# Optimization experiments

Measured on AMD Instinct MI355X. Metric: run time of the kernel, lower is better.

## Reference

```python
import jax, jax.numpy as jnp
import numpy as np

B = 262144
D = 16
G = 20000


def setup_inputs() -> dict:
    key = jax.random.key(0)
    ks = jax.random.split(key, 20)
    lin = lambda k, o, i: jax.random.normal(k, (o, i), jnp.float32) * (1.0 / np.sqrt(i))
    inp = {
        "x": jax.random.randint(ks[0], (B, 2), 0, G),
        "phenos": jax.random.normal(ks[1], (B, 2), jnp.float32),
        "emb": jax.random.normal(ks[2], (G, D), jnp.float32),
        "W1": lin(ks[3], D, D), "b1": jnp.zeros((D,), jnp.float32),
        "W2": lin(ks[4], D, D), "b2": jnp.zeros((D,), jnp.float32),
        "W3": lin(ks[5], D, D), "b3": jnp.zeros((D,), jnp.float32),
        # bilinear weights: small noise + stacked identity, as in the torch init
        "BW": 0.01 * jax.random.normal(ks[6], (D, D, D), jnp.float32)
              + jnp.broadcast_to(jnp.eye(D, dtype=jnp.float32)[None, :, :], (D, D, D)),
        "BD": 0.01 * jax.random.normal(ks[7], (D, D), jnp.float32) + 1.0,
        "Boff": 0.01 * jax.random.normal(ks[8], (D,), jnp.float32),
        "Wc1": lin(ks[9], D, D), "bc1": jnp.zeros((D,), jnp.float32),
        "Wc2": lin(ks[10], 1, D), "bc2": jnp.zeros((1,), jnp.float32),
    }
    return inp


def reference(x, phenos, emb, W1, b1, W2, b2, W3, b3, BW, BD, Boff, Wc1, bc1, Wc2, bc2):
    # embedding lookup: [B, 2, D] -> flatten gene axis into batch
    h = emb[x].reshape(-1, D)
    # embedding_ffn (dropout is identity in eval): Linear->ReLU->Linear->ReLU->Linear
    h = jax.nn.relu(h @ W1.T + b1)
    h = jax.nn.relu(h @ W2.T + b2)
    h = (h @ W3.T + b3).reshape(-1, 2, D)
    e0, e1 = h[:, 0, :], h[:, 1, :]  # [B, D] each
    # torch: x0 = BW.matmul(e0.T).T  -> x0[b,m,n] = sum_k BW[n,m,k] e0[b,k]
    A = jnp.einsum("nmk,bk->bmn", BW, e0)  # [B, D, D]
    # torch: x1 = BW.matmul(e1.T).T, *= BD, permute -> C[b,m,n] = sum_k BW[m,n,k] e1[b,k], scaled by BD[n,m]
    C = jnp.einsum("mnk,bk->bmn", BW, e1)  # [B, D, D]
    z = jnp.einsum("bmn,bmn,nm->bn", A, C, BD) + Boff  # [B, D]
    # embedding_comb: Linear->ReLU->Linear(D,1)
    z = jax.nn.relu(z @ Wc1.T + bc1)
    z = z @ Wc2.T + bc2  # [B, 1]
    return jnp.sum(phenos, axis=1) + z[:, 0]
```

## Files before the change

### kernel.cpp

```cpp
#include <hip/hip_runtime.h>

#define D  16
#define NB 262144
#define NG 20000

typedef __attribute__((ext_vector_type(8))) short bf16x8;
typedef __attribute__((ext_vector_type(4))) float f32x4;

__device__ __forceinline__ unsigned pack_hi16(unsigned b0, unsigned b1) {
    return __builtin_amdgcn_perm(b1, b0, 0x07060302u);
}

__global__ void build_kernel(const float* __restrict__ BW, const float* __restrict__ BD,
                             const float* __restrict__ Wc1, const float* __restrict__ bc1,
                             const float* __restrict__ Boff,
                             short* __restrict__ Bhi, short* __restrict__ Blo,
                             float* __restrict__ bc1p) {
    __shared__ float bw[4096];
    __shared__ float bd[256];
    __shared__ float M[256][16];
    int tid = threadIdx.x;
    #pragma unroll
    for (int i = 0; i < 16; ++i) bw[tid + 256 * i] = BW[tid + 256 * i];
    bd[tid] = BD[tid];
    __syncthreads();

    int k = tid >> 4, j = tid & 15;
    #pragma unroll
    for (int n = 0; n < 16; ++n) {
        float acc = 0.f;
        #pragma unroll
        for (int m = 0; m < 16; ++m)
            acc += bd[n * 16 + m] * bw[(n * 16 + m) * 16 + k] * bw[(m * 16 + n) * 16 + j];
        M[tid][n] = acc;
    }
    __syncthreads();

    for (int idx = tid; idx < 512; idx += 256) {
        int s = idx >> 6, lane = idx & 63;
        int q = lane >> 4, n = lane & 15;
        unsigned hw[4], lw[4];
        #pragma unroll
        for (int w = 0; w < 4; ++w) {
            int kk0 = s * 32 + q * 8 + 2 * w;
            float v0 = M[kk0][n], v1 = M[kk0 + 1][n];
            unsigned b0 = __float_as_uint(v0), b1 = __float_as_uint(v1);
            float h0 = __uint_as_float(b0 & 0xFFFF0000u);
            float h1 = __uint_as_float(b1 & 0xFFFF0000u);
            hw[w] = pack_hi16(b0, b1);
            lw[w] = pack_hi16(__float_as_uint(v0 - h0), __float_as_uint(v1 - h1));
        }
        uint4* bh4 = (uint4*)Bhi;
        uint4* bl4 = (uint4*)Blo;
        bh4[idx] = make_uint4(hw[0], hw[1], hw[2], hw[3]);
        bl4[idx] = make_uint4(lw[0], lw[1], lw[2], lw[3]);
    }

    if (tid < 16) {
        float a = bc1[tid];
        #pragma unroll
        for (int n = 0; n < 16; ++n) a += Wc1[tid * 16 + n] * Boff[n];
        bc1p[tid] = a;
    }
}

__global__ void gene_mlp_kernel(const float* __restrict__ emb,
                                const float* __restrict__ W1, const float* __restrict__ b1,
                                const float* __restrict__ W2, const float* __restrict__ b2,
                                const float* __restrict__ W3, const float* __restrict__ b3,
                                float* __restrict__ T) {
    int g = blockIdx.x * blockDim.x + threadIdx.x;
    if (g >= NG) return;

    float h[D], t[D];
    const float4* ep = (const float4*)(emb + (size_t)g * D);
    float4 v0 = ep[0], v1 = ep[1], v2 = ep[2], v3 = ep[3];
    h[0]=v0.x; h[1]=v0.y; h[2]=v0.z; h[3]=v0.w;
    h[4]=v1.x; h[5]=v1.y; h[6]=v1.z; h[7]=v1.w;
    h[8]=v2.x; h[9]=v2.y; h[10]=v2.z; h[11]=v2.w;
    h[12]=v3.x; h[13]=v3.y; h[14]=v3.z; h[15]=v3.w;

    #pragma unroll
    for (int i = 0; i < D; ++i) {
        float a = b1[i];
        #pragma unroll
        for (int d = 0; d < D; ++d) a = fmaf(W1[i * D + d], h[d], a);
        t[i] = fmaxf(a, 0.f);
    }
    #pragma unroll
    for (int i = 0; i < D; ++i) {
        float a = b2[i];
        #pragma unroll
        for (int d = 0; d < D; ++d) a = fmaf(W2[i * D + d], t[d], a);
        h[i] = fmaxf(a, 0.f);
    }
    #pragma unroll
    for (int i = 0; i < D; ++i) {
        float a = b3[i];
        #pragma unroll
        for (int d = 0; d < D; ++d) a = fmaf(W3[i * D + d], h[d], a);
        t[i] = a;
    }

    float4* tp = (float4*)(T + (size_t)g * D);
    tp[0] = make_float4(t[0], t[1], t[2], t[3]);
    tp[1] = make_float4(t[4], t[5], t[6], t[7]);
    tp[2] = make_float4(t[8], t[9], t[10], t[11]);
    tp[3] = make_float4(t[12], t[13], t[14], t[15]);
}

__global__ void __launch_bounds__(256, 2)
main_kernel(const int* __restrict__ x, const float* __restrict__ phenos,
            const float* __restrict__ T,
            const short* __restrict__ Bhi, const short* __restrict__ Blo,
            const float* __restrict__ bc1p, const float* __restrict__ Wc1,
            const float* __restrict__ Wc2, const float* __restrict__ bc2,
            float* __restrict__ out) {
    int tid  = threadIdx.x;
    int wave = tid >> 6, lane = tid & 63;
    int quad = lane >> 4, nl = lane & 15;
    long base = (long)blockIdx.x * 256 + wave * 64;

    bf16x8 bh[8], bl[8];
    #pragma unroll
    for (int s = 0; s < 8; ++s) {
        bh[s] = ((const bf16x8*)Bhi)[s * 64 + lane];
        bl[s] = ((const bf16x8*)Blo)[s * 64 + lane];
    }

    f32x4 acc[4];
    #pragma unroll
    for (int t = 0; t < 4; ++t) acc[t] = (f32x4){0.f, 0.f, 0.f, 0.f};

    const int c_add = quad >> 1;
    const int e1off = (quad & 1) * 8;

    #pragma unroll
    for (int t = 0; t < 4; ++t) {
        long r = base + t * 16 + nl;
        int2 g = ((const int2*)x)[r];

        const f32x4* p0 = (const f32x4*)(T + g.x * 16);
        const f32x4* p1 = (const f32x4*)(T + g.y * 16 + e1off);
        f32x4 a0 = p0[0], a1 = p0[1], a2 = p0[2], a3 = p0[3];
        f32x4 c0 = p1[0], c1 = p1[1];
        float e0[16] = {a0.x,a0.y,a0.z,a0.w, a1.x,a1.y,a1.z,a1.w,
                        a2.x,a2.y,a2.z,a2.w, a3.x,a3.y,a3.z,a3.w};
        float e1v[8] = {c0.x,c0.y,c0.z,c0.w, c1.x,c1.y,c1.z,c1.w};

        float ev[8];
        #pragma unroll
        for (int s = 0; s < 8; ++s) ev[s] = c_add ? e0[2 * s + 1] : e0[2 * s];

        #pragma unroll
        for (int s = 0; s < 8; ++s) {
            unsigned hb[8];
            float lo[8];
            #pragma unroll
            for (int jj = 0; jj < 8; ++jj) {
                float p = ev[s] * e1v[jj];
                unsigned b = __float_as_uint(p);
                hb[jj] = b;
                lo[jj] = p - __uint_as_float(b & 0xFFFF0000u);
            }
            uint4 aw = make_uint4(pack_hi16(hb[0], hb[1]), pack_hi16(hb[2], hb[3]),
                                  pack_hi16(hb[4], hb[5]), pack_hi16(hb[6], hb[7]));
            uint4 lw = make_uint4(
                pack_hi16(__float_as_uint(lo[0]), __float_as_uint(lo[1])),
                pack_hi16(__float_as_uint(lo[2]), __float_as_uint(lo[3])),
                pack_hi16(__float_as_uint(lo[4]), __float_as_uint(lo[5])),
                pack_hi16(__float_as_uint(lo[6]), __float_as_uint(lo[7])));
            bf16x8 ah = __builtin_bit_cast(bf16x8, aw);
            bf16x8 al = __builtin_bit_cast(bf16x8, lw);
            acc[t] = __builtin_amdgcn_mfma_f32_16x16x32_bf16(ah, bh[s], acc[t], 0, 0, 0);
            acc[t] = __builtin_amdgcn_mfma_f32_16x16x32_bf16(ah, bl[s], acc[t], 0, 0, 0);
            acc[t] = __builtin_amdgcn_mfma_f32_16x16x32_bf16(al, bh[s], acc[t], 0, 0, 0);
        }
    }

    __shared__ float zbuf[4][16][65];
    #pragma unroll
    for (int t = 0; t < 4; ++t) {
        #pragma unroll
        for (int reg = 0; reg < 4; ++reg)
            zbuf[wave][nl][t * 16 + quad * 4 + reg] = acc[t][reg];
    }
    __syncthreads();

    float zv[16];
    #pragma unroll
    for (int n = 0; n < 16; ++n) zv[n] = zbuf[wave][n][lane];

    float a2 = bc2[0];
    #pragma unroll
    for (int i = 0; i < 16; ++i) {
        float u = bc1p[i];
        #pragma unroll
        for (int n = 0; n < 16; ++n) u = fmaf(Wc1[i * 16 + n], zv[n], u);
        u = fmaxf(u, 0.f);
        a2 = fmaf(Wc2[i], u, a2);
    }

    long r2 = base + lane;
    float2 ph = ((const float2*)phenos)[r2];
    out[r2] = ph.x + ph.y + a2;
}

extern "C" void kernel_launch(void* const* d_in, const int* in_sizes, int n_in,
                              void* d_out, int out_size, void* d_ws, size_t ws_size,
                              hipStream_t stream) {
    const int*   x      = (const int*)  d_in[0];
    const float* phenos = (const float*)d_in[1];
    const float* emb    = (const float*)d_in[2];
    const float* W1     = (const float*)d_in[3];
    const float* b1     = (const float*)d_in[4];
    const float* W2     = (const float*)d_in[5];
    const float* b2     = (const float*)d_in[6];
    const float* W3     = (const float*)d_in[7];
    const float* b3     = (const float*)d_in[8];
    const float* BW     = (const float*)d_in[9];
    const float* BD     = (const float*)d_in[10];
    const float* Boff   = (const float*)d_in[11];
    const float* Wc1    = (const float*)d_in[12];
    const float* bc1    = (const float*)d_in[13];
    const float* Wc2    = (const float*)d_in[14];
    const float* bc2    = (const float*)d_in[15];
    float* out = (float*)d_out;

    char* wsb = (char*)d_ws;
    short* Bhi = (short*)(wsb);
    short* Blo = (short*)(wsb + 8192);
    float* bc1p = (float*)(wsb + 16384);
    float* T    = (float*)(wsb + 16448);

    build_kernel<<<1, 256, 0, stream>>>(BW, BD, Wc1, bc1, Boff, Bhi, Blo, bc1p);
    gene_mlp_kernel<<<(NG + 255) / 256, 256, 0, stream>>>(emb, W1, b1, W2, b2, W3, b3, T);
    main_kernel<<<NB / 256, 256, 0, stream>>>(x, phenos, T, Bhi, Blo, bc1p, Wc1, Wc2, bc2, out);
}
```

Baseline: 126.7 us.

## Merge prep kernels and stage gathered embedding rows through shared memory

Combines the single-block bilinear build and the gene MLP into one launch, with the last block doing the build, which removes one kernel launch and overlaps the serial build with the MLP. The build now accumulates 16 outputs per thread using vectorized shared-memory reads. In the main kernel each lane gathers both T rows for its own batch row once, with coalesced-per-lane loads, and writes them to padded LDS. The MFMA operand construction then reads from LDS instead of issuing redundant per-quad global gathers. The product split is also written as packed float2 ops, at the cost of more LDS traffic and extra barriers.

```diff
diff --git a/kernel.cpp b/kernel.cpp
--- a/kernel.cpp
+++ b/kernel.cpp
@@ -3,123 +3,138 @@
 #define D  16
 #define NB 262144
 #define NG 20000
+#define ROWPITCH 36
 
 typedef __attribute__((ext_vector_type(8))) short bf16x8;
 typedef __attribute__((ext_vector_type(4))) float f32x4;
+typedef __attribute__((ext_vector_type(2))) float f32x2;
+typedef __attribute__((ext_vector_type(2))) unsigned u32x2;
 
 __device__ __forceinline__ unsigned pack_hi16(unsigned b0, unsigned b1) {
     return __builtin_amdgcn_perm(b1, b0, 0x07060302u);
 }
 
-__global__ void build_kernel(const float* __restrict__ BW, const float* __restrict__ BD,
-                             const float* __restrict__ Wc1, const float* __restrict__ bc1,
-                             const float* __restrict__ Boff,
-                             short* __restrict__ Bhi, short* __restrict__ Blo,
-                             float* __restrict__ bc1p) {
-    __shared__ float bw[4096];
-    __shared__ float bd[256];
-    __shared__ float M[256][16];
+__global__ void __launch_bounds__(256)
+prep_kernel(const float* __restrict__ emb,
+            const float* __restrict__ W1, const float* __restrict__ b1,
+            const float* __restrict__ W2, const float* __restrict__ b2,
+            const float* __restrict__ W3, const float* __restrict__ b3,
+            const float* __restrict__ BW, const float* __restrict__ BD,
+            const float* __restrict__ Wc1, const float* __restrict__ bc1,
+            const float* __restrict__ Boff,
+            float* __restrict__ T, short* __restrict__ Bhi, short* __restrict__ Blo,
+            float* __restrict__ bc1p) {
+    __shared__ float smem[8704];
     int tid = threadIdx.x;
-    #pragma unroll
-    for (int i = 0; i < 16; ++i) bw[tid + 256 * i] = BW[tid + 256 * i];
-    bd[tid] = BD[tid];
-    __syncthreads();
-
-    int k = tid >> 4, j = tid & 15;
-    #pragma unroll
-    for (int n = 0; n < 16; ++n) {
-        float acc = 0.f;
-        #pragma unroll
-        for (int m = 0; m < 16; ++m)
-            acc += bd[n * 16 + m] * bw[(n * 16 + m) * 16 + k] * bw[(m * 16 + n) * 16 + j];
-        M[tid][n] = acc;
-    }
+    int blk = blockIdx.x;
+
+    if (blk < 79) {
+        int g = blk * 256 + tid;
+        if (g >= NG) return;
+        float h[D], t[D];
+        const float4* ep = (const float4*)(emb + (size_t)g * D);
+        float4 v0 = ep[0], v1 = ep[1], v2 = ep[2], v3 = ep[3];
+        h[0]=v0.x; h[1]=v0.y; h[2]=v0.z; h[3]=v0.w;
+        h[4]=v1.x; h[5]=v1.y; h[6]=v1.z; h[7]=v1.w;
+        h[8]=v2.x; h[9]=v2.y; h[10]=v2.z; h[11]=v2.w;
+        h[12]=v3.x; h[13]=v3.y; h[14]=v3.z; h[15]=v3.w;
+        #pragma unroll
+        for (int i = 0; i < D; ++i) {
+            float a = b1[i];
+            #pragma unroll
+            for (int d = 0; d < D; ++d) a = fmaf(W1[i * D + d], h[d], a);
+            t[i] = fmaxf(a, 0.f);
+        }
+        #pragma unroll
+        for (int i = 0; i < D; ++i) {
+            float a = b2[i];
+            #pragma unroll
+            for (int d = 0; d < D; ++d) a = fmaf(W2[i * D + d], t[d], a);
+            h[i] = fmaxf(a, 0.f);
+        }
+        #pragma unroll
+        for (int i = 0; i < D; ++i) {
+            float a = b3[i];
+            #pragma unroll
+            for (int d = 0; d < D; ++d) a = fmaf(W3[i * D + d], h[d], a);
+            t[i] = a;
+        }
+        float4* tp = (float4*)(T + (size_t)g * D);
+        tp[0] = make_float4(t[0], t[1], t[2], t[3]);
+        tp[1] = make_float4(t[4], t[5], t[6], t[7]);
+        tp[2] = make_float4(t[8], t[9], t[10], t[11]);
+        tp[3] = make_float4(t[12], t[13], t[14], t[15]);
+        return;
+    }
+
+    float* bwS = smem;
+    float* bdS = smem + 4096;
+    float* MmS = smem + 4352;
+    #pragma unroll
+    for (int i = 0; i < 16; ++i) bwS[tid + 256 * i] = BW[tid + 256 * i];
+    bdS[tid] = BD[tid];
+    __syncthreads();
+
+    int n = tid >> 4, j = tid & 15;
+    float acc[16];
+    #pragma unroll
+    for (int k = 0; k < 16; ++k) acc[k] = 0.f;
+    #pragma unroll
+    for (int m = 0; m < 16; ++m) {
+        float sw = bdS[n * 16 + m] * bwS[(m * 16 + n) * 16 + j];
+        const f32x4* w1 = (const f32x4*)&bwS[(n * 16 + m) * 16];
+        #pragma unroll
+        for (int q = 0; q < 4; ++q) {
+            f32x4 w = w1[q];
+            acc[4 * q + 0] = fmaf(sw, w.x, acc[4 * q + 0]);
+            acc[4 * q + 1] = fmaf(sw, w.y, acc[4 * q + 1]);
+            acc[4 * q + 2] = fmaf(sw, w.z, acc[4 * q + 2]);
+            acc[4 * q + 3] = fmaf(sw, w.w, acc[4 * q + 3]);
+        }
+    }
+    #pragma unroll
+    for (int k = 0; k < 16; ++k) MmS[(k * 16 + j) * 17 + n] = acc[k];
     __syncthreads();
 
     for (int idx = tid; idx < 512; idx += 256) {
         int s = idx >> 6, lane = idx & 63;
-        int q = lane >> 4, n = lane & 15;
+        int q = lane >> 4, nn = lane & 15;
         unsigned hw[4], lw[4];
         #pragma unroll
         for (int w = 0; w < 4; ++w) {
             int kk0 = s * 32 + q * 8 + 2 * w;
-            float v0 = M[kk0][n], v1 = M[kk0 + 1][n];
+            float v0 = MmS[kk0 * 17 + nn], v1 = MmS[(kk0 + 1) * 17 + nn];
             unsigned b0 = __float_as_uint(v0), b1 = __float_as_uint(v1);
             float h0 = __uint_as_float(b0 & 0xFFFF0000u);
             float h1 = __uint_as_float(b1 & 0xFFFF0000u);
             hw[w] = pack_hi16(b0, b1);
             lw[w] = pack_hi16(__float_as_uint(v0 - h0), __float_as_uint(v1 - h1));
         }
-        uint4* bh4 = (uint4*)Bhi;
-        uint4* bl4 = (uint4*)Blo;
-        bh4[idx] = make_uint4(hw[0], hw[1], hw[2], hw[3]);
-        bl4[idx] = make_uint4(lw[0], lw[1], lw[2], lw[3]);
+        ((uint4*)Bhi)[idx] = make_uint4(hw[0], hw[1], hw[2], hw[3]);
+        ((uint4*)Blo)[idx] = make_uint4(lw[0], lw[1], lw[2], lw[3]);
     }
 
     if (tid < 16) {
         float a = bc1[tid];
         #pragma unroll
-        for (int n = 0; n < 16; ++n) a += Wc1[tid * 16 + n] * Boff[n];
+        for (int nn = 0; nn < 16; ++nn) a += Wc1[tid * 16 + nn] * Boff[nn];
         bc1p[tid] = a;
     }
 }
 
-__global__ void gene_mlp_kernel(const float* __restrict__ emb,
-                                const float* __restrict__ W1, const float* __restrict__ b1,
-                                const float* __restrict__ W2, const float* __restrict__ b2,
-                                const float* __restrict__ W3, const float* __restrict__ b3,
-                                float* __restrict__ T) {
-    int g = blockIdx.x * blockDim.x + threadIdx.x;
-    if (g >= NG) return;
-
-    float h[D], t[D];
-    const float4* ep = (const float4*)(emb + (size_t)g * D);
-    float4 v0 = ep[0], v1 = ep[1], v2 = ep[2], v3 = ep[3];
-    h[0]=v0.x; h[1]=v0.y; h[2]=v0.z; h[3]=v0.w;
-    h[4]=v1.x; h[5]=v1.y; h[6]=v1.z; h[7]=v1.w;
-    h[8]=v2.x; h[9]=v2.y; h[10]=v2.z; h[11]=v2.w;
-    h[12]=v3.x; h[13]=v3.y; h[14]=v3.z; h[15]=v3.w;
-
-    #pragma unroll
-    for (int i = 0; i < D; ++i) {
-        float a = b1[i];
-        #pragma unroll
-        for (int d = 0; d < D; ++d) a = fmaf(W1[i * D + d], h[d], a);
-        t[i] = fmaxf(a, 0.f);
-    }
-    #pragma unroll
-    for (int i = 0; i < D; ++i) {
-        float a = b2[i];
-        #pragma unroll
-        for (int d = 0; d < D; ++d) a = fmaf(W2[i * D + d], t[d], a);
-        h[i] = fmaxf(a, 0.f);
-    }
-    #pragma unroll
-    for (int i = 0; i < D; ++i) {
-        float a = b3[i];
-        #pragma unroll
-        for (int d = 0; d < D; ++d) a = fmaf(W3[i * D + d], h[d], a);
-        t[i] = a;
-    }
-
-    float4* tp = (float4*)(T + (size_t)g * D);
-    tp[0] = make_float4(t[0], t[1], t[2], t[3]);
-    tp[1] = make_float4(t[4], t[5], t[6], t[7]);
-    tp[2] = make_float4(t[8], t[9], t[10], t[11]);
-    tp[3] = make_float4(t[12], t[13], t[14], t[15]);
-}
-
-__global__ void __launch_bounds__(256, 2)
+__global__ void __launch_bounds__(256)
 main_kernel(const int* __restrict__ x, const float* __restrict__ phenos,
             const float* __restrict__ T,
             const short* __restrict__ Bhi, const short* __restrict__ Blo,
             const float* __restrict__ bc1p, const float* __restrict__ Wc1,
             const float* __restrict__ Wc2, const float* __restrict__ bc2,
             float* __restrict__ out) {
+    __shared__ float smem[9216];
     int tid  = threadIdx.x;
     int wave = tid >> 6, lane = tid & 63;
     int quad = lane >> 4, nl = lane & 15;
     long base = (long)blockIdx.x * 256 + wave * 64;
+    float* stg = smem + wave * 2304;
 
     bf16x8 bh[8], bl[8];
     #pragma unroll
@@ -128,68 +143,71 @@
         bl[s] = ((const bf16x8*)Blo)[s * 64 + lane];
     }
 
+    long r = base + lane;
+    int2 g = ((const int2*)x)[r];
+    {
+        const f32x4* p0 = (const f32x4*)(T + g.x * 16);
+        const f32x4* p1 = (const f32x4*)(T + g.y * 16);
+        f32x4 c0 = p0[0], c1 = p0[1], c2 = p0[2], c3 = p0[3];
+        f32x4 c4 = p1[0], c5 = p1[1], c6 = p1[2], c7 = p1[3];
+        f32x4* wp = (f32x4*)(stg + lane * ROWPITCH);
+        wp[0] = c0; wp[1] = c1; wp[2] = c2; wp[3] = c3;
+        wp[4] = c4; wp[5] = c5; wp[6] = c6; wp[7] = c7;
+    }
+    __syncthreads();
+
     f32x4 acc[4];
     #pragma unroll
     for (int t = 0; t < 4; ++t) acc[t] = (f32x4){0.f, 0.f, 0.f, 0.f};
-
-    const int c_add = quad >> 1;
-    const int e1off = (quad & 1) * 8;
+    const int par = quad >> 1;
+    const int eo  = (quad & 1) * 8;
 
     #pragma unroll
     for (int t = 0; t < 4; ++t) {
-        long r = base + t * 16 + nl;
-        int2 g = ((const int2*)x)[r];
-
-        const f32x4* p0 = (const f32x4*)(T + g.x * 16);
-        const f32x4* p1 = (const f32x4*)(T + g.y * 16 + e1off);
-        f32x4 a0 = p0[0], a1 = p0[1], a2 = p0[2], a3 = p0[3];
-        f32x4 c0 = p1[0], c1 = p1[1];
-        float e0[16] = {a0.x,a0.y,a0.z,a0.w, a1.x,a1.y,a1.z,a1.w,
-                        a2.x,a2.y,a2.z,a2.w, a3.x,a3.y,a3.z,a3.w};
-        float e1v[8] = {c0.x,c0.y,c0.z,c0.w, c1.x,c1.y,c1.z,c1.w};
-
+        const float* rowp = stg + (t * 16 + nl) * ROWPITCH;
         float ev[8];
         #pragma unroll
-        for (int s = 0; s < 8; ++s) ev[s] = c_add ? e0[2 * s + 1] : e0[2 * s];
+        for (int s = 0; s < 8; ++s) ev[s] = rowp[2 * s + par];
+        f32x4 e1a = *(const f32x4*)(rowp + 16 + eo);
+        f32x4 e1b = *(const f32x4*)(rowp + 20 + eo);
+        f32x2 e1p[4] = {(f32x2){e1a.x, e1a.y}, (f32x2){e1a.z, e1a.w},
+                        (f32x2){e1b.x, e1b.y}, (f32x2){e1b.z, e1b.w}};
 
         #pragma unroll
         for (int s = 0; s < 8; ++s) {
-            unsigned hb[8];
-            float lo[8];
-            #pragma unroll
-            for (int jj = 0; jj < 8; ++jj) {
-                float p = ev[s] * e1v[jj];
-                unsigned b = __float_as_uint(p);
-                hb[jj] = b;
-                lo[jj] = p - __uint_as_float(b & 0xFFFF0000u);
+            f32x2 evv = (f32x2){ev[s], ev[s]};
+            unsigned aw[4], lw[4];
+            #pragma unroll
+            for (int w = 0; w < 4; ++w) {
+                f32x2 p  = evv * e1p[w];
+                u32x2 pb = __builtin_bit_cast(u32x2, p);
+                u32x2 hb = pb & (u32x2){0xFFFF0000u, 0xFFFF0000u};
+                f32x2 lo = p - __builtin_bit_cast(f32x2, hb);
+                u32x2 lb = __builtin_bit_cast(u32x2, lo);
+                aw[w] = pack_hi16(pb.x, pb.y);
+                lw[w] = pack_hi16(lb.x, lb.y);
             }
-            uint4 aw = make_uint4(pack_hi16(hb[0], hb[1]), pack_hi16(hb[2], hb[3]),
-                                  pack_hi16(hb[4], hb[5]), pack_hi16(hb[6], hb[7]));
-            uint4 lw = make_uint4(
-                pack_hi16(__float_as_uint(lo[0]), __float_as_uint(lo[1])),
-                pack_hi16(__float_as_uint(lo[2]), __float_as_uint(lo[3])),
-                pack_hi16(__float_as_uint(lo[4]), __float_as_uint(lo[5])),
-                pack_hi16(__float_as_uint(lo[6]), __float_as_uint(lo[7])));
-            bf16x8 ah = __builtin_bit_cast(bf16x8, aw);
-            bf16x8 al = __builtin_bit_cast(bf16x8, lw);
+            bf16x8 ah = __builtin_bit_cast(bf16x8, make_uint4(aw[0], aw[1], aw[2], aw[3]));
+            bf16x8 al = __builtin_bit_cast(bf16x8, make_uint4(lw[0], lw[1], lw[2], lw[3]));
             acc[t] = __builtin_amdgcn_mfma_f32_16x16x32_bf16(ah, bh[s], acc[t], 0, 0, 0);
             acc[t] = __builtin_amdgcn_mfma_f32_16x16x32_bf16(ah, bl[s], acc[t], 0, 0, 0);
             acc[t] = __builtin_amdgcn_mfma_f32_16x16x32_bf16(al, bh[s], acc[t], 0, 0, 0);
         }
     }
 
-    __shared__ float zbuf[4][16][65];
+    __syncthreads();
+    float* zb = smem + wave * 1040;
     #pragma unroll
     for (int t = 0; t < 4; ++t) {
         #pragma unroll
         for (int reg = 0; reg < 4; ++reg)
-            zbuf[wave][nl][t * 16 + quad * 4 + reg] = acc[t][reg];
+            zb[nl * 65 + t * 16 + quad * 4 + reg] = acc[t][reg];
     }
     __syncthreads();
 
     float zv[16];
     #pragma unroll
-    for (int n = 0; n < 16; ++n) zv[n] = zbuf[wave][n][lane];
+    for (int n = 0; n < 16; ++n) zv[n] = zb[n * 65 + lane];
 
     float a2 = bc2[0];
     #pragma unroll
@@ -201,9 +219,8 @@
         a2 = fmaf(Wc2[i], u, a2);
     }
 
-    long r2 = base + lane;
-    float2 ph = ((const float2*)phenos)[r2];
-    out[r2] = ph.x + ph.y + a2;
+    float2 ph = ((const float2*)phenos)[r];
+    out[r] = ph.x + ph.y + a2;
 }
 
 extern "C" void kernel_launch(void* const* d_in, const int* in_sizes, int n_in,
@@ -228,12 +245,12 @@
     float* out = (float*)d_out;
 
     char* wsb = (char*)d_ws;
-    short* Bhi = (short*)(wsb);
-    short* Blo = (short*)(wsb + 8192);
+    short* Bhi  = (short*)(wsb);
+    short* Blo  = (short*)(wsb + 8192);
     float* bc1p = (float*)(wsb + 16384);
     float* T    = (float*)(wsb + 16448);
 
-    build_kernel<<<1, 256, 0, stream>>>(BW, BD, Wc1, bc1, Boff, Bhi, Blo, bc1p);
-    gene_mlp_kernel<<<(NG + 255) / 256, 256, 0, stream>>>(emb, W1, b1, W2, b2, W3, b3, T);
+    prep_kernel<<<80, 256, 0, stream>>>(emb, W1, b1, W2, b2, W3, b3, BW, BD,
+                                        Wc1, bc1, Boff, T, Bhi, Blo, bc1p);
     main_kernel<<<NB / 256, 256, 0, stream>>>(x, phenos, T, Bhi, Blo, bc1p, Wc1, Wc2, bc2, out);
 }
```

Result: faster. 112.8 us (-11.0%).
